# Kernel optimization log

Hardware: AMD Instinct MI355X
Metric: run time of the kernel (lower is better)

## Reference

```python
import jax, jax.numpy as jnp
import numpy as np
from jax.scipy.special import logsumexp

WORD_DIM = 512
SCRF_DIM = 256
N_TAGS = 12
ALLOWED_SPAN = 8
START_ID = 10
STOP_ID = 11
SEQ_LEN = 768
N_SPANS = 96


def _compute_scores(h, Wl, bl, Wr, br, Gl, bgl, Gr, bgr, Wt, bt, transitions):
    # h: [1, L, D] already projected by Dense
    Lc, D = h.shape[1], h.shape[2]
    scores = jnp.zeros((1, Lc, Lc, D), h.dtype)
    diag = jnp.arange(Lc)
    ht = h
    scores = scores.at[:, diag, diag].set(ht)
    for sl in range(1, min(ALLOWED_SPAN, Lc)):
        l, r = ht[:, :-1], ht[:, 1:]
        h_hat = 4.0 * jax.nn.sigmoid(l @ Wl.T + bl + r @ Wr.T + br) - 2.0
        # exp/normalize over 3 gates == softmax over gate axis
        g = (l @ Gl.T + bgl + r @ Gr.T + bgr).reshape(1, Lc - sl, 3, D)
        wgt = jax.nn.softmax(g, axis=2)
        ht = wgt[:, :, 0] * h_hat + wgt[:, :, 1] * l + wgt[:, :, 2] * r
        scores = scores.at[:, diag[:Lc - sl], diag[sl:]].set(ht)
    tagsc = scores @ Wt.T + bt  # [1, L, L, T]
    # final[b,i,j,prev,tag] = tagsc[b,i,j,tag] + transitions[prev,tag]
    return tagsc[:, :, :, None, :] + transitions[None, None, None]


def _forward_pass(s5):
    # s5: [1, L, L, T, T]; semi-Markov forward algorithm, windows of width <= ALLOWED_SPAN
    Lc, T = s5.shape[1], s5.shape[3]
    A = ALLOWED_SPAN
    i0 = jnp.arange(1, Lc + 1)
    k = jnp.arange(A)
    p = i0[:, None] - A + k[None, :]              # candidate span-start positions [L, A]
    m = p >= 0                                    # valid window mask (istarts = max(0, i-A))
    x = s5[0][jnp.clip(p, 0), (i0 - 1)[:, None]]  # [L, A, T, T] span scores ending at i-1
    buf0 = jnp.full((A, T), -10000.0, s5.dtype).at[A - 1, START_ID].set(0.0)

    def step(buf, inp):
        xi, mi = inp
        # tmp[k, prev, tag] = score + logalpha[start, prev]
        tmp = jnp.where(mi[:, None, None], xi + buf[:, :, None], -1e30)
        na = logsumexp(tmp, axis=(0, 1))  # [T]
        return jnp.concatenate([buf[1:], na[None]], axis=0), na

    _, alphas = jax.lax.scan(step, buf0, (x, m))
    return alphas[-1, :STOP_ID].sum()


def _gold_score(s5, tags):
    Lc, T = s5.shape[1], s5.shape[3]
    gf = tags[:, :, 0] * (Lc * T * T) + tags[:, :, 1] * (T * T) + tags[:, :, 2] * T + tags[:, :, 3]
    return jnp.take_along_axis(s5.reshape(1, -1), gf, axis=1).sum()


def setup_inputs() -> dict:
    key = jax.random.key(0)
    ks = jax.random.split(key, 16)
    D, W3 = SCRF_DIM, 3 * SCRF_DIM
    s = 0.05
    def w(k, shape):
        return jax.random.normal(k, shape, dtype=jnp.float32) * s
    return {
        "feats": jax.random.normal(ks[0], (1, SEQ_LEN, WORD_DIM), dtype=jnp.float32),
        "tags": jax.random.randint(ks[1], (1, N_SPANS, 4), 0, N_TAGS),
        "Wd": w(ks[2], (D, WORD_DIM)), "bd": jnp.zeros((D,), jnp.float32),
        "Wl": w(ks[3], (D, D)), "bl": jnp.zeros((D,), jnp.float32),
        "Wr": w(ks[4], (D, D)), "br": jnp.zeros((D,), jnp.float32),
        "Gl": w(ks[5], (W3, D)), "bgl": jnp.zeros((W3,), jnp.float32),
        "Gr": w(ks[6], (W3, D)), "bgr": jnp.zeros((W3,), jnp.float32),
        "Wt": w(ks[7], (N_TAGS, D)), "bt": jnp.zeros((N_TAGS,), jnp.float32),
        "transitions": w(ks[8], (N_TAGS, N_TAGS)),
    }


def reference(feats, tags, Wd, bd, Wl, bl, Wr, br, Gl, bgl, Gr, bgr, Wt, bt, transitions):
    h = feats @ Wd.T + bd  # Dense: word_dim -> scrf_dim
    s5 = _compute_scores(h, Wl, bl, Wr, br, Gl, bgl, Gr, bgr, Wt, bt, transitions)
    gold = _gold_score(s5, tags)
    logZ = _forward_pass(s5)
    return logZ - gold
```

## Files before the change

kernel.cpp:

```cpp
#include <hip/hip_runtime.h>

typedef __attribute__((ext_vector_type(8))) short short8;
typedef __attribute__((ext_vector_type(4))) float f32x4;

#define TPAD 100

__device__ __forceinline__ float bf2f(short s) {
  return __uint_as_float(((unsigned)(unsigned short)s) << 16);
}
__device__ __forceinline__ unsigned short f2bf(float f) {
  unsigned u = __float_as_uint(f);
  unsigned rounding = 0x7fffu + ((u >> 16) & 1u);
  return (unsigned short)((u + rounding) >> 16);
}

struct F8 { float4 a, b; };
__device__ __forceinline__ F8 ldf8(const float* p) {
  F8 r; r.a = *(const float4*)p; r.b = *(const float4*)(p + 4); return r;
}
__device__ __forceinline__ short8 cvtF8(F8 v) {
  short8 r;
  r[0]=(short)f2bf(v.a.x); r[1]=(short)f2bf(v.a.y); r[2]=(short)f2bf(v.a.z); r[3]=(short)f2bf(v.a.w);
  r[4]=(short)f2bf(v.b.x); r[5]=(short)f2bf(v.b.y); r[6]=(short)f2bf(v.b.z); r[7]=(short)f2bf(v.b.w);
  return r;
}

__device__ __forceinline__ void stg_f32(float* p, float v) {
  asm volatile("global_store_dword %0, %1, off sc1" :: "v"(p), "v"(v) : "memory");
}
__device__ __forceinline__ void stg_u16(unsigned short* p, unsigned short v) {
  unsigned w = v;
  asm volatile("global_store_short %0, %1, off sc1" :: "v"(p), "v"(w) : "memory");
}
__device__ __forceinline__ void stg_u32(unsigned* p, unsigned v) {
  asm volatile("global_store_dword %0, %1, off sc1" :: "v"(p), "v"(v) : "memory");
}

#define NFLAGS 18432
__device__ __forceinline__ void flag_spin(unsigned* f, unsigned tgt) {
  unsigned n = 0;
  while (__hip_atomic_load(f, __ATOMIC_RELAXED, __HIP_MEMORY_SCOPE_AGENT) < tgt) {
    __builtin_amdgcn_s_sleep(1);
    if (++n > 2000000u) break;
  }
}
#define DRAIN() asm volatile("s_waitcnt vmcnt(0) lgkmcnt(0)" ::: "memory")
#define KTBAR() do { \
  asm volatile("s_waitcnt lgkmcnt(0)" ::: "memory"); \
  __builtin_amdgcn_s_barrier(); \
  __builtin_amdgcn_sched_barrier(0); \
} while (0)

union __align__(16) SmemU {
  struct { unsigned short As[2][64][72]; unsigned short Ws[2][64][72]; float Cs[64][64]; } g;
  struct { unsigned short rows[2][8][264]; float sred[2][96]; float smu[2]; } bn;
  struct { float Bs[96 * TPAD]; float Acs[96 * TPAD]; float red[8]; } t;
  struct { float Qs[2][96 * TPAD]; float vv[4][96]; float red[8]; float redm[4]; } f;
};

__global__ void prep_kernel(const float* __restrict__ bl, const float* __restrict__ br,
                            const float* __restrict__ bgl, const float* __restrict__ bgr,
                            float* __restrict__ bc, unsigned* __restrict__ flags)
{
  int idx = blockIdx.x * 256 + threadIdx.x;
  if (idx < 1024) {
    bc[idx] = (idx < 256) ? bl[idx] + br[idx] : bgl[idx-256] + bgr[idx-256];
  } else {
    int j = idx - 1024;
    if (j < NFLAGS) flags[j] = 0u;
  }
}

__device__ __forceinline__ void treelevel(SmemU& sm,
    const float* Tin, const float* Cin, float* Tout, float* Cout)
{
  const int bid = blockIdx.x;
  const int tid = threadIdx.x;
  const int wv = tid >> 6, lane = tid & 63;
  const int j = bid >> 1;
  const int cs = (bid & 1) * 48;
  const float* Ag = Tin + (size_t)(2*j) * 9216;
  const float* Bg = Tin + (size_t)(2*j + 1) * 9216;

  float4 av[9], bv[9];
  const float* ap = Ag + tid * 36;
  const float* bp = Bg + tid * 36;
  #pragma unroll
  for (int q = 0; q < 9; ++q) av[q] = *(const float4*)(ap + q*4);
  #pragma unroll
  for (int q = 0; q < 9; ++q) bv[q] = *(const float4*)(bp + q*4);
  float ma = 0.f, mb = 0.f;
  #pragma unroll
  for (int q = 0; q < 9; ++q) {
    ma = fmaxf(ma, fmaxf(fmaxf(av[q].x, av[q].y), fmaxf(av[q].z, av[q].w)));
    mb = fmaxf(mb, fmaxf(fmaxf(bv[q].x, bv[q].y), fmaxf(bv[q].z, bv[q].w)));
  }
  #pragma unroll
  for (int off = 32; off; off >>= 1) {
    ma = fmaxf(ma, __shfl_down(ma, off));
    mb = fmaxf(mb, __shfl_down(mb, off));
  }
  if (lane == 0) { sm.t.red[wv] = ma; sm.t.red[4 + wv] = mb; }
  __syncthreads();
  float fa = fmaxf(fmaxf(sm.t.red[0], sm.t.red[1]), fmaxf(sm.t.red[2], sm.t.red[3]));
  float fb = fmaxf(fmaxf(sm.t.red[4], sm.t.red[5]), fmaxf(sm.t.red[6], sm.t.red[7]));
  float ia = 1.0f / fa, ib = 1.0f / fb;

  #pragma unroll
  for (int q = 0; q < 9; ++q) {
    int e = tid*36 + q*4;
    int r = e / 96, k = e - r*96;
    float4 bb = bv[q];
    bb.x *= ib; bb.y *= ib; bb.z *= ib; bb.w *= ib;
    *(float4*)&sm.t.Bs[r*TPAD + k] = bb;
    float4 aa = av[q];
    sm.t.Acs[(k+0)*TPAD + r] = aa.x * ia;
    sm.t.Acs[(k+1)*TPAD + r] = aa.y * ia;
    sm.t.Acs[(k+2)*TPAD + r] = aa.z * ia;
    sm.t.Acs[(k+3)*TPAD + r] = aa.w * ia;
  }
  __syncthreads();

  int tr = tid >> 4, tc = tid & 15;
  int r0 = tr * 6, c0 = cs + tc * 3;
  float acc[6][3];
  #pragma unroll
  for (int i = 0; i < 6; ++i)
    #pragma unroll
    for (int m = 0; m < 3; ++m) acc[i][m] = 0.f;
  for (int k = 0; k < 96; k += 4) {
    float4 a0 = *(const float4*)&sm.t.Acs[(c0+0)*TPAD + k];
    float4 a1 = *(const float4*)&sm.t.Acs[(c0+1)*TPAD + k];
    float4 a2 = *(const float4*)&sm.t.Acs[(c0+2)*TPAD + k];
    #pragma unroll
    for (int i = 0; i < 6; ++i) {
      float4 b = *(const float4*)&sm.t.Bs[(r0+i)*TPAD + k];
      acc[i][0] += b.x*a0.x + b.y*a0.y + b.z*a0.z + b.w*a0.w;
      acc[i][1] += b.x*a1.x + b.y*a1.y + b.z*a1.z + b.w*a1.w;
      acc[i][2] += b.x*a2.x + b.y*a2.y + b.z*a2.z + b.w*a2.w;
    }
  }
  float* op = Tout + (size_t)j * 9216;
  #pragma unroll
  for (int i = 0; i < 6; ++i)
    #pragma unroll
    for (int m = 0; m < 3; ++m)
      stg_f32(&op[(size_t)(r0+i)*96 + c0 + m], acc[i][m]);
  if ((bid & 1) == 0 && tid == 0)
    stg_f32(&Cout[j], Cin[2*j] + Cin[2*j + 1] + __logf(fa) + __logf(fb));
}

__global__ __launch_bounds__(256, 1) void mega_kernel(
    const float* feats, const float* Wd, const float* bd,
    const float* Wl, const float* Wr, const float* Gl, const float* Gr,
    unsigned short* WcB, const float* bc,
    unsigned short* ht, const float* Wt, const float* bt,
    float* Bband, float* Xn, float* muv, const float* trans,
    const int* tags,
    float* T0, float* T1, float* T2, float* T3, float* T4,
    float* C0, float* C1, float* C2, float* C3, float* C4,
    float* out, unsigned* flags)
{
  __shared__ SmemU sm;
  const int bid = blockIdx.x;
  const int tid = threadIdx.x;
  const int wave = tid >> 6, lane = tid & 63;

  if (bid >= 48) {
    for (int j = (bid - 48)*256 + tid; j < 524288; j += 208*256) {
      int o = j >> 9, k = j & 511;
      float v;
      if (k < 256) v = (o < 256) ? Wl[o*256 + k] : Gl[(o-256)*256 + k];
      else { int k2 = k - 256; v = (o < 256) ? Wr[o*256 + k2] : Gr[(o-256)*256 + k2]; }
      stg_u16(&WcB[j], f2bf(v));
    }
    DRAIN();
    __syncthreads();
    if (tid == 0) atomicAdd(&flags[573*32], 1u);
  }

  if (bid < 192) {
    const int p = bid % 12;
    const int lr = tid >> 3;
    const int c8 = (tid & 7) * 8;
    if (bid < 48) {
      const int p0 = p * 64;
      const int n0 = (bid / 12) * 64;
      f32x4 acc[4];
      #pragma unroll
      for (int i = 0; i < 4; ++i)
        #pragma unroll
        for (int j = 0; j < 4; ++j) acc[i][j] = 0.f;
      F8 fa0[2], fa1[2], fw0[2], fw1[2];
      #pragma unroll
      for (int q = 0; q < 2; ++q) {
        int kb = q * 64;
        fa0[q] = ldf8(feats + (size_t)(p0 + lr)*512 + kb + c8);
        fa1[q] = ldf8(feats + (size_t)(p0 + lr + 32)*512 + kb + c8);
        fw0[q] = ldf8(Wd + (size_t)(n0 + lr)*512 + kb + c8);
        fw1[q] = ldf8(Wd + (size_t)(n0 + lr + 32)*512 + kb + c8);
      }
      #pragma unroll
      for (int kt = 0; kt < 8; ++kt) {
        const int sb = kt & 1;
        *(short8*)(&sm.g.As[sb][lr][c8])      = cvtF8(fa0[sb]);
        *(short8*)(&sm.g.As[sb][lr + 32][c8]) = cvtF8(fa1[sb]);
        *(short8*)(&sm.g.Ws[sb][lr][c8])      = cvtF8(fw0[sb]);
        *(short8*)(&sm.g.Ws[sb][lr + 32][c8]) = cvtF8(fw1[sb]);
        if (kt < 6) {
          int kb = (kt + 2) * 64;
          fa0[sb] = ldf8(feats + (size_t)(p0 + lr)*512 + kb + c8);
          fa1[sb] = ldf8(feats + (size_t)(p0 + lr + 32)*512 + kb + c8);
          fw0[sb] = ldf8(Wd + (size_t)(n0 + lr)*512 + kb + c8);
          fw1[sb] = ldf8(Wd + (size_t)(n0 + lr + 32)*512 + kb + c8);
        }
        KTBAR();
        int q8 = (lane >> 4) * 8;
        #pragma unroll
        for (int kk = 0; kk < 2; ++kk) {
          short8 bfr = *(const short8*)(&sm.g.Ws[sb][wave*16 + (lane & 15)][kk*32 + q8]);
          #pragma unroll
          for (int mt = 0; mt < 4; ++mt) {
            short8 afr = *(const short8*)(&sm.g.As[sb][mt*16 + (lane & 15)][kk*32 + q8]);
            acc[mt] = __builtin_amdgcn_mfma_f32_16x16x32_bf16(afr, bfr, acc[mt], 0, 0, 0);
          }
        }
        KTBAR();
      }
      int o = n0 + wave*16 + (lane & 15);
      float bias = bd[o];
      #pragma unroll
      for (int mt = 0; mt < 4; ++mt)
        #pragma unroll
        for (int r = 0; r < 4; ++r) {
          int row = p0 + mt*16 + (lane >> 4)*4 + r;
          stg_u16(&ht[row*256 + o], f2bf(acc[mt][r] + bias));
        }
      DRAIN();
      __syncthreads();
      if (tid == 0) atomicAdd(&flags[(0*12 + p)*32], 1u);
    }

    const int p0 = p * 64;
    const int n0i = (bid / 12) * 16;
    const int o0w = (lr >> 4)*256 + n0i + (lr & 15);
    const int o1w = ((lr+32) >> 4)*256 + n0i + ((lr+32) & 15);
    for (int sl = 1; sl <= 7; ++sl) {
      if (sl == 1) {
        if (tid == 0) flag_spin(&flags[573*32], 208u);
        __syncthreads();
      }
      short8 sw0[2], sw1[2], sa0[2], sa1[2];
      #pragma unroll
      for (int q = 0; q < 2; ++q) {
        int kb = q * 64;
        sw0[q] = *(const short8*)(WcB + (size_t)o0w*512 + kb + c8);
        sw1[q] = *(const short8*)(WcB + (size_t)o1w*512 + kb + c8);
      }
      unsigned tgt = (sl == 1) ? 4u : 16u;
      if (tid == 0) {
        flag_spin(&flags[((sl-1)*12 + p)*32], tgt);
        if (p < 11) flag_spin(&flags[((sl-1)*12 + p + 1)*32], tgt);
      }
      __syncthreads();
      {
        const unsigned short* htp = ht + (size_t)(sl - 1) * 196608;
        unsigned short* htn = ht + (size_t)sl * 196608;
        const int Mvalid = 768 - sl;
        f32x4 acc[4];
        #pragma unroll
        for (int i = 0; i < 4; ++i)
          #pragma unroll
          for (int j = 0; j < 4; ++j) acc[i][j] = 0.f;
        #pragma unroll
        for (int q = 0; q < 2; ++q) {
          int kb = q * 64;
          int g0 = p0 + lr;      if (g0 > 767) g0 = 767;
          int g1 = p0 + lr + 32; if (g1 > 767) g1 = 767;
          sa0[q] = *(const short8*)(htp + (size_t)g0*256 + kb + c8);
          sa1[q] = *(const short8*)(htp + (size_t)g1*256 + kb + c8);
        }
        #pragma unroll
        for (int kt = 0; kt < 8; ++kt) {
          const int sb = kt & 1;
          *(short8*)(&sm.g.As[sb][lr][c8])      = sa0[sb];
          *(short8*)(&sm.g.As[sb][lr + 32][c8]) = sa1[sb];
          *(short8*)(&sm.g.Ws[sb][lr][c8])      = sw0[sb];
          *(short8*)(&sm.g.Ws[sb][lr + 32][c8]) = sw1[sb];
          if (kt < 6) {
            int kb = (kt + 2) * 64;
            int shift = kb >> 8;
            int kcol = kb & 255;
            int g0 = p0 + lr + shift;      if (g0 > 767) g0 = 767;
            int g1 = p0 + lr + 32 + shift; if (g1 > 767) g1 = 767;
            sa0[sb] = *(const short8*)(htp + (size_t)g0*256 + kcol + c8);
            sa1[sb] = *(const short8*)(htp + (size_t)g1*256 + kcol + c8);
            sw0[sb] = *(const short8*)(WcB + (size_t)o0w*512 + kb + c8);
            sw1[sb] = *(const short8*)(WcB + (size_t)o1w*512 + kb + c8);
          }
          KTBAR();
          int q8 = (lane >> 4) * 8;
          #pragma unroll
          for (int kk = 0; kk < 2; ++kk) {
            short8 bfr = *(const short8*)(&sm.g.Ws[sb][wave*16 + (lane & 15)][kk*32 + q8]);
            #pragma unroll
            for (int mt = 0; mt < 4; ++mt) {
              short8 afr = *(const short8*)(&sm.g.As[sb][mt*16 + (lane & 15)][kk*32 + q8]);
              acc[mt] = __builtin_amdgcn_mfma_f32_16x16x32_bf16(afr, bfr, acc[mt], 0, 0, 0);
            }
          }
          KTBAR();
        }
        #pragma unroll
        for (int mt = 0; mt < 4; ++mt)
          #pragma unroll
          for (int r = 0; r < 4; ++r)
            sm.g.Cs[mt*16 + (lane >> 4)*4 + r][wave*16 + (lane & 15)] = acc[mt][r];
        __syncthreads();

        int dl = tid & 7;
        int d0 = n0i + dl*2;
        int cc0 = dl*2;
        float bz0 = bc[d0],       bz1 = bc[d0+1];
        float b00 = bc[256 + d0], b01 = bc[256 + d0 + 1];
        float b10 = bc[512 + d0], b11 = bc[512 + d0 + 1];
        float b20 = bc[768 + d0], b21 = bc[768 + d0 + 1];
        for (int pr = tid >> 3; pr < 64; pr += 32) {
          int pw = p0 + pr;
          if (pw >= Mvalid) continue;
          float z0 = sm.g.Cs[pr][cc0]      + bz0, z1 = sm.g.Cs[pr][cc0+1]      + bz1;
          float g00 = sm.g.Cs[pr][16+cc0]  + b00, g01 = sm.g.Cs[pr][16+cc0+1]  + b01;
          float g10 = sm.g.Cs[pr][32+cc0]  + b10, g11 = sm.g.Cs[pr][32+cc0+1]  + b11;
          float g20 = sm.g.Cs[pr][48+cc0]  + b20, g21 = sm.g.Cs[pr][48+cc0+1]  + b21;
          unsigned lv = *(const unsigned*)(htp + (size_t)pw*256 + d0);
          unsigned rv = *(const unsigned*)(htp + (size_t)(pw+1)*256 + d0);
          float l0 = bf2f((short)(lv & 0xffff)), l1 = bf2f((short)(lv >> 16));
          float r0v = bf2f((short)(rv & 0xffff)), r1v = bf2f((short)(rv >> 16));
          float hh0 = 4.f / (1.f + __expf(-z0)) - 2.f;
          float hh1 = 4.f / (1.f + __expf(-z1)) - 2.f;
          float mg0 = fmaxf(g00, fmaxf(g10, g20));
          float mg1 = fmaxf(g01, fmaxf(g11, g21));
          float e00 = __expf(g00 - mg0), e10 = __expf(g10 - mg0), e20 = __expf(g20 - mg0);
          float e01 = __expf(g01 - mg1), e11 = __expf(g11 - mg1), e21 = __expf(g21 - mg1);
          float o0 = (e00*hh0 + e10*l0 + e20*r0v) / (e00 + e10 + e20);
          float o1 = (e01*hh1 + e11*l1 + e21*r1v) / (e01 + e11 + e21);
          unsigned pack = (unsigned)f2bf(o0) | ((unsigned)f2bf(o1) << 16);
          stg_u32((unsigned*)(htn + (size_t)pw*256 + d0), pack);
        }
      }
      DRAIN();
      __syncthreads();
      if (tid == 0) atomicAdd(&flags[(sl*12 + p)*32], 1u);
    }
  }

  for (int task = bid; task < 384; task += 256) {
    if (tid == 0) {
      int rlo = 2*task - 7; if (rlo < 0) rlo = 0;
      int tlo = rlo >> 6, thi = (2*task + 1) >> 6;
      flag_spin(&flags[(7*12 + tlo)*32], 16u);
      if (thi != tlo) flag_spin(&flags[(7*12 + thi)*32], 16u);
    }
    __syncthreads();
    const int half = tid >> 7;
    const int t2 = tid & 127;
    const int i = 2*task + 1 + half;
    for (int q = t2; q < 256; q += 128) {
      int k = q >> 5, cc = (q & 31) * 8;
      int pr = i - 8 + k;
      short8 v;
      if (pr >= 0) {
        int slx = 7 - k;
        v = *(const short8*)(ht + ((size_t)slx*768 + pr)*256 + cc);
      } else {
        #pragma unroll
        for (int j = 0; j < 8; ++j) v[j] = 0;
      }
      *(short8*)(&sm.bn.rows[half][k][cc]) = v;
    }
    __syncthreads();
    float res = -1e30f;
    if (t2 < 96) {
      int t = t2 >> 3, k = t2 & 7;
      int pr = i - 8 + k;
      if (pr >= 0) {
        float acc = 0.f;
        for (int dch = 0; dch < 256; dch += 8) {
          float4 wa = *(const float4*)(Wt + t*256 + dch);
          float4 wb = *(const float4*)(Wt + t*256 + dch + 4);
          short8 hv = *(const short8*)(&sm.bn.rows[half][k][dch]);
          acc += wa.x*bf2f(hv[0]) + wa.y*bf2f(hv[1]) + wa.z*bf2f(hv[2]) + wa.w*bf2f(hv[3])
               + wb.x*bf2f(hv[4]) + wb.y*bf2f(hv[5]) + wb.z*bf2f(hv[6]) + wb.w*bf2f(hv[7]);
        }
        res = acc + bt[t];
      }
      stg_f32(&Bband[(size_t)i*96 + t2], res);
      sm.bn.sred[half][t2] = res;
    }
    __syncthreads();
    if (t2 < 32) {
      float m = fmaxf(sm.bn.sred[half][t2],
                 fmaxf(sm.bn.sred[half][t2+32], sm.bn.sred[half][t2+64]));
      #pragma unroll
      for (int off = 16; off; off >>= 1) m = fmaxf(m, __shfl_down(m, off));
      if (t2 == 0) { stg_f32(&muv[i], m); sm.bn.smu[half] = m; }
    }
    __syncthreads();
    if (t2 < 96) stg_f32(&Xn[(size_t)i*96 + t2], __expf(res - sm.bn.smu[half]));
    DRAIN();
    __syncthreads();
    if (tid == 0) atomicAdd(&flags[(96 + task)*32], 1u);
  }
  if (bid >= 240) return;

  {
    const int chunk = bid / 5;
    const int bxx = bid % 5;
    if (tid == 0) {
      #pragma unroll
      for (int q = 0; q < 8; ++q)
        flag_spin(&flags[(96 + 8*chunk + q)*32], 1u);
    }
    __syncthreads();
    if (bxx == 0 && tid == 0) stg_f32(&C0[chunk], 0.f);
    const int a = chunk * 16;
    const int g = lane / 12;
    const int t = lane - g * 12;
    const int cidx = bxx * 20 + wave * 5 + g;
    const bool active = (g < 5) && (cidx < 96);
    const int c = active ? cidx : 95;
    const int s = c / 12, tau = c - s * 12;
    float Etc[12];
    #pragma unroll
    for (int jj = 0; jj < 12; ++jj) Etc[jj] = __expf(trans[jj*12 + t]);
    float NA[8], V[8];
    #pragma unroll
    for (int jj = 0; jj < 8; ++jj) { NA[jj] = 0.f; V[jj] = 0.f; }
    #pragma unroll
    for (int jj = 0; jj < 8; ++jj) if (jj == s) {
      NA[jj] = (t == tau) ? 1.f : 0.f;
      V[jj]  = Etc[tau];
    }
    const int gbb = (g * 12) * 4;
    #pragma unroll
    for (int m = 1; m <= 16; ++m) {
      const float* xr = Xn + (size_t)(a + m) * 96 + t * 8;
      float4 x0 = *(const float4*)xr;
      float4 x1 = *(const float4*)(xr + 4);
      float sf = __expf(-muv[a + m]);
      float na = x0.x*V[0] + x0.y*V[1] + x0.z*V[2] + x0.w*V[3]
               + x1.x*V[4] + x1.y*V[5] + x1.z*V[6] + x1.w*V[7];
      int nai = __float_as_int(na);
      float nb[12];
      #pragma unroll
      for (int jj = 0; jj < 12; ++jj)
        nb[jj] = __int_as_float(__builtin_amdgcn_ds_bpermute(gbb + jj*4, nai));
      float pp0 = nb[0]*Etc[0] + nb[1]*Etc[1] + nb[2]*Etc[2]   + nb[3]*Etc[3];
      float pp1 = nb[4]*Etc[4] + nb[5]*Etc[5] + nb[6]*Etc[6]   + nb[7]*Etc[7];
      float pp2 = nb[8]*Etc[8] + nb[9]*Etc[9] + nb[10]*Etc[10] + nb[11]*Etc[11];
      float v = (pp0 + pp1) + pp2;
      #pragma unroll
      for (int kq = 0; kq < 7; ++kq) { NA[kq] = NA[kq+1]*sf; V[kq] = V[kq+1]*sf; }
      NA[7] = na; V[7] = v;
    }
    if (active) {
      float* dst = T0 + (size_t)chunk * 9216 + c;
      #pragma unroll
      for (int jj = 0; jj < 8; ++jj) stg_f32(&dst[(size_t)(jj*12 + t) * 96], NA[jj]);
    }
    DRAIN();
    __syncthreads();
    if (tid == 0) atomicAdd(&flags[(480 + chunk)*32], 1u);
  }
  if (bid >= 48) return;

  {
    int j = bid >> 1;
    if (tid == 0) {
      flag_spin(&flags[(480 + 2*j    )*32], 5u);
      flag_spin(&flags[(480 + 2*j + 1)*32], 5u);
    }
    __syncthreads();
    treelevel(sm, T0, C0, T1, C1);
    DRAIN(); __syncthreads();
    if (tid == 0) atomicAdd(&flags[(528 + j)*32], 1u);
  }
  if (bid >= 24) return;
  {
    int j = bid >> 1;
    if (tid == 0) {
      flag_spin(&flags[(528 + 2*j    )*32], 2u);
      flag_spin(&flags[(528 + 2*j + 1)*32], 2u);
    }
    __syncthreads();
    treelevel(sm, T1, C1, T2, C2);
    DRAIN(); __syncthreads();
    if (tid == 0) atomicAdd(&flags[(552 + j)*32], 1u);
  }
  if (bid >= 12) return;
  {
    int j = bid >> 1;
    if (tid == 0) {
      flag_spin(&flags[(552 + 2*j    )*32], 2u);
      flag_spin(&flags[(552 + 2*j + 1)*32], 2u);
    }
    __syncthreads();
    treelevel(sm, T2, C2, T3, C3);
    DRAIN(); __syncthreads();
    if (tid == 0) atomicAdd(&flags[(564 + j)*32], 1u);
  }
  if (bid >= 6) return;
  {
    int j = bid >> 1;
    if (tid == 0) {
      flag_spin(&flags[(564 + 2*j    )*32], 2u);
      flag_spin(&flags[(564 + 2*j + 1)*32], 2u);
    }
    __syncthreads();
    treelevel(sm, T3, C3, T4, C4);
    DRAIN(); __syncthreads();
    if (tid == 0) atomicAdd(&flags[(570 + j)*32], 1u);
  }
  if (bid) return;

  {
    if (tid == 0) {
      flag_spin(&flags[(570)*32], 2u);
      flag_spin(&flags[(571)*32], 2u);
      flag_spin(&flags[(572)*32], 2u);
    }
    __syncthreads();
    float4 P[9];
    const float* p0p = T4 + tid * 36;
    #pragma unroll
    for (int q = 0; q < 9; ++q) P[q] = *(const float4*)(p0p + q*4);

    float gold = 0.f;
    if (tid < 96) {
      int a = tags[tid*4+0], b = tags[tid*4+1], cc = tags[tid*4+2], d = tags[tid*4+3];
      float v = trans[cc*12 + d];
      int sl = b - a;
      if (sl >= 0 && sl < 8) v += Bband[(size_t)(b+1)*96 + d*8 + (7 - sl)];
      else v += bt[d];
      gold = v;
    }
    float mp = 0.f;
    for (int q = tid; q < 768; q += 256) mp += muv[1 + q];
    #pragma unroll
    for (int off = 32; off; off >>= 1) {
      gold += __shfl_down(gold, off);
      mp   += __shfl_down(mp, off);
    }
    if (lane == 0) { sm.f.red[wave] = gold; sm.f.red[4 + wave] = mp; }

    #pragma unroll
    for (int q = 0; q < 9; ++q) {
      int e = tid*36 + q*4;
      int r = e / 96, k = e - r*96;
      *(float4*)&sm.f.Qs[0][r*TPAD + k] = P[q];
    }
    if (tid < 96) sm.f.vv[0][tid] = (tid == 94) ? 1.f : 0.f;
    __syncthreads();
    float gold_t = sm.f.red[0] + sm.f.red[1] + sm.f.red[2] + sm.f.red[3];
    float musum  = sm.f.red[4] + sm.f.red[5] + sm.f.red[6] + sm.f.red[7];
    float Ct = C4[0] + C4[1] + C4[2];

    #pragma unroll
    for (int s = 0; s < 3; ++s) {
      if (s < 2) {
        const float* pn = T4 + (size_t)(s+1)*9216 + tid*36;
        #pragma unroll
        for (int q = 0; q < 9; ++q) P[q] = *(const float4*)(pn + q*4);
      }
      float acc = 0.f;
      if (tid < 96) {
        const float* Qr = &sm.f.Qs[s & 1][tid * TPAD];
        #pragma unroll
        for (int k = 0; k < 96; k += 4) {
          float4 qv = *(const float4*)(Qr + k);
          float4 zv = *(const float4*)&sm.f.vv[s][k];
          acc += qv.x*zv.x + qv.y*zv.y + qv.z*zv.z + qv.w*zv.w;
        }
      }
      float am = (tid < 96) ? acc : 0.f;
      #pragma unroll
      for (int off = 32; off; off >>= 1) am = fmaxf(am, __shfl_down(am, off));
      if (lane == 0) sm.f.redm[wave] = am;
      __syncthreads();
      float mx = fmaxf(fmaxf(sm.f.redm[0], sm.f.redm[1]), fmaxf(sm.f.redm[2], sm.f.redm[3]));
      Ct += __logf(mx);
      if (tid < 96) sm.f.vv[s+1][tid] = acc / mx;
      if (s < 2) {
        #pragma unroll
        for (int q = 0; q < 9; ++q) {
          int e = tid*36 + q*4;
          int r = e / 96, k = e - r*96;
          *(float4*)&sm.f.Qs[(s+1)&1][r*TPAD + k] = P[q];
        }
      }
      __syncthreads();
    }
    if (tid == 0) {
      float lsum = 0.f;
      #pragma unroll
      for (int t = 0; t < 11; ++t) lsum += __logf(sm.f.vv[3][84 + t]);
      out[0] = lsum + 11.f * (Ct + musum) - gold_t;
    }
  }
}

extern "C" void kernel_launch(void* const* d_in, const int* in_sizes, int n_in,
                              void* d_out, int out_size, void* d_ws, size_t ws_size,
                              hipStream_t stream)
{
  const float* feats = (const float*)d_in[0];
  const int*   tags  = (const int*)  d_in[1];
  const float* Wd    = (const float*)d_in[2];
  const float* bd    = (const float*)d_in[3];
  const float* Wl    = (const float*)d_in[4];
  const float* bl    = (const float*)d_in[5];
  const float* Wr    = (const float*)d_in[6];
  const float* br    = (const float*)d_in[7];
  const float* Gl    = (const float*)d_in[8];
  const float* bgl   = (const float*)d_in[9];
  const float* Gr    = (const float*)d_in[10];
  const float* bgr   = (const float*)d_in[11];
  const float* Wt    = (const float*)d_in[12];
  const float* bt    = (const float*)d_in[13];
  const float* trans = (const float*)d_in[14];
  float* out = (float*)d_out;

  char* ws = (char*)d_ws;
  unsigned short* WcB    = (unsigned short*)(ws + 1048576);
  float*          bc     = (float*)         (ws + 2097152);
  unsigned short* ht     = (unsigned short*)(ws + 2101248);
  float*          Bband  = (float*)         (ws + 5246976);
  float*          Xn     = (float*)         (ws + 5542272);
  float*          muv    = (float*)         (ws + 5837568);
  float*          T0     = (float*)         (ws + 5841664);
  float*          T1     = (float*)         (ws + 7611136);
  float*          T2     = (float*)         (ws + 8495872);
  float*          T3     = (float*)         (ws + 8938240);
  float*          T4     = (float*)         (ws + 9159424);
  float*          C0     = (float*)         (ws + 9270016);
  float*          C1     = (float*)         (ws + 9270272);
  float*          C2     = (float*)         (ws + 9270528);
  float*          C3     = (float*)         (ws + 9270784);
  float*          C4     = (float*)         (ws + 9271040);
  unsigned*       flags  = (unsigned*)      (ws + 9271296);

  prep_kernel<<<76, 256, 0, stream>>>(bl, br, bgl, bgr, bc, flags);
  mega_kernel<<<256, 256, 0, stream>>>(feats, Wd, bd, Wl, Wr, Gl, Gr, WcB, bc,
                                       ht, Wt, bt, Bband, Xn, muv, trans, tags,
                                       T0, T1, T2, T3, T4, C0, C1, C2, C3, C4,
                                       out, flags);
}
```

Measured before the change: 204.1 us.

## Keep span-GEMM weight fragments in registers and read activations directly from global

Before the span-level loop, each wave now loads all of its weight fragments for the combined gate/hidden GEMM into registers once and keeps them across all seven span lengths, instead of reloading them from global memory every level. The A-operand activations are read straight from global memory into MFMA fragments, which removes the double-buffered LDS staging and its per-k-tile barriers. Launch bounds change to allow two blocks per CU. The goal is less redundant weight traffic and fewer synchronisations. The cost is higher register pressure from 16 short8 fragments, more uncoalesced direct global loads for activations, and a possible conflict between the register demand and the 2-blocks launch bound.

```diff
diff --git a/kernel.cpp b/kernel.cpp
--- a/kernel.cpp
+++ b/kernel.cpp
@@ -150,7 +150,7 @@
     stg_f32(&Cout[j], Cin[2*j] + Cin[2*j + 1] + __logf(fa) + __logf(fb));
 }
 
-__global__ __launch_bounds__(256, 1) void mega_kernel(
+__global__ __launch_bounds__(256, 2) void mega_kernel(
     const float* feats, const float* Wd, const float* bd,
     const float* Wl, const float* Wr, const float* Gl, const float* Gr,
     unsigned short* WcB, const float* bc,
@@ -243,81 +243,57 @@
 
     const int p0 = p * 64;
     const int n0i = (bid / 12) * 16;
-    const int o0w = (lr >> 4)*256 + n0i + (lr & 15);
-    const int o1w = ((lr+32) >> 4)*256 + n0i + ((lr+32) & 15);
+    const int q8 = (lane >> 4) * 8;
+    if (tid == 0) flag_spin(&flags[573*32], 208u);
+    __syncthreads();
+    short8 wfrag[16];
+    {
+      const size_t wrow = (size_t)(wave*256 + n0i + (lane & 15)) * 512;
+      #pragma unroll
+      for (int kt = 0; kt < 8; ++kt)
+        #pragma unroll
+        for (int kk = 0; kk < 2; ++kk)
+          wfrag[kt*2 + kk] = *(const short8*)(WcB + wrow + kt*64 + kk*32 + q8);
+    }
     for (int sl = 1; sl <= 7; ++sl) {
-      if (sl == 1) {
-        if (tid == 0) flag_spin(&flags[573*32], 208u);
-        __syncthreads();
-      }
-      short8 sw0[2], sw1[2], sa0[2], sa1[2];
-      #pragma unroll
-      for (int q = 0; q < 2; ++q) {
-        int kb = q * 64;
-        sw0[q] = *(const short8*)(WcB + (size_t)o0w*512 + kb + c8);
-        sw1[q] = *(const short8*)(WcB + (size_t)o1w*512 + kb + c8);
-      }
       unsigned tgt = (sl == 1) ? 4u : 16u;
       if (tid == 0) {
         flag_spin(&flags[((sl-1)*12 + p)*32], tgt);
         if (p < 11) flag_spin(&flags[((sl-1)*12 + p + 1)*32], tgt);
       }
       __syncthreads();
-      {
-        const unsigned short* htp = ht + (size_t)(sl - 1) * 196608;
-        unsigned short* htn = ht + (size_t)sl * 196608;
-        const int Mvalid = 768 - sl;
-        f32x4 acc[4];
-        #pragma unroll
-        for (int i = 0; i < 4; ++i)
-          #pragma unroll
-          for (int j = 0; j < 4; ++j) acc[i][j] = 0.f;
-        #pragma unroll
-        for (int q = 0; q < 2; ++q) {
-          int kb = q * 64;
-          int g0 = p0 + lr;      if (g0 > 767) g0 = 767;
-          int g1 = p0 + lr + 32; if (g1 > 767) g1 = 767;
-          sa0[q] = *(const short8*)(htp + (size_t)g0*256 + kb + c8);
-          sa1[q] = *(const short8*)(htp + (size_t)g1*256 + kb + c8);
-        }
-        #pragma unroll
-        for (int kt = 0; kt < 8; ++kt) {
-          const int sb = kt & 1;
-          *(short8*)(&sm.g.As[sb][lr][c8])      = sa0[sb];
-          *(short8*)(&sm.g.As[sb][lr + 32][c8]) = sa1[sb];
-          *(short8*)(&sm.g.Ws[sb][lr][c8])      = sw0[sb];
-          *(short8*)(&sm.g.Ws[sb][lr + 32][c8]) = sw1[sb];
-          if (kt < 6) {
-            int kb = (kt + 2) * 64;
-            int shift = kb >> 8;
-            int kcol = kb & 255;
-            int g0 = p0 + lr + shift;      if (g0 > 767) g0 = 767;
-            int g1 = p0 + lr + 32 + shift; if (g1 > 767) g1 = 767;
-            sa0[sb] = *(const short8*)(htp + (size_t)g0*256 + kcol + c8);
-            sa1[sb] = *(const short8*)(htp + (size_t)g1*256 + kcol + c8);
-            sw0[sb] = *(const short8*)(WcB + (size_t)o0w*512 + kb + c8);
-            sw1[sb] = *(const short8*)(WcB + (size_t)o1w*512 + kb + c8);
-          }
-          KTBAR();
-          int q8 = (lane >> 4) * 8;
+      const unsigned short* htp = ht + (size_t)(sl - 1) * 196608;
+      unsigned short* htn = ht + (size_t)sl * 196608;
+      const int Mvalid = 768 - sl;
+      f32x4 acc[4];
+      #pragma unroll
+      for (int i = 0; i < 4; ++i)
+        #pragma unroll
+        for (int j = 0; j < 4; ++j) acc[i][j] = 0.f;
+      #pragma unroll
+      for (int kt = 0; kt < 8; ++kt) {
+        const int kcol = (kt & 3) * 64;
+        const int shift = kt >> 2;
+        #pragma unroll
+        for (int mt = 0; mt < 4; ++mt) {
+          int grow = p0 + mt*16 + (lane & 15) + shift;
+          if (grow > 767) grow = 767;
+          const unsigned short* ap = htp + (size_t)grow*256 + kcol + q8;
           #pragma unroll
           for (int kk = 0; kk < 2; ++kk) {
-            short8 bfr = *(const short8*)(&sm.g.Ws[sb][wave*16 + (lane & 15)][kk*32 + q8]);
-            #pragma unroll
-            for (int mt = 0; mt < 4; ++mt) {
-              short8 afr = *(const short8*)(&sm.g.As[sb][mt*16 + (lane & 15)][kk*32 + q8]);
-              acc[mt] = __builtin_amdgcn_mfma_f32_16x16x32_bf16(afr, bfr, acc[mt], 0, 0, 0);
-            }
+            short8 afr = *(const short8*)(ap + kk*32);
+            acc[mt] = __builtin_amdgcn_mfma_f32_16x16x32_bf16(afr, wfrag[kt*2 + kk], acc[mt], 0, 0, 0);
           }
-          KTBAR();
-        }
-        #pragma unroll
-        for (int mt = 0; mt < 4; ++mt)
-          #pragma unroll
-          for (int r = 0; r < 4; ++r)
-            sm.g.Cs[mt*16 + (lane >> 4)*4 + r][wave*16 + (lane & 15)] = acc[mt][r];
-        __syncthreads();
-
+        }
+      }
+      #pragma unroll
+      for (int mt = 0; mt < 4; ++mt)
+        #pragma unroll
+        for (int r = 0; r < 4; ++r)
+          sm.g.Cs[mt*16 + (lane >> 4)*4 + r][wave*16 + (lane & 15)] = acc[mt][r];
+      __syncthreads();
+
+      {
         int dl = tid & 7;
         int d0 = n0i + dl*2;
         int cc0 = dl*2;
```

After: 238.6 us. +16.9%, slower.
